# Performance work log

Hardware: AMD Instinct MI355X
Metric: run time of the kernel (lower is better)

## Reference

```python
import jax, jax.numpy as jnp
import numpy as np

B, T, D = 2, 4096, 2048
HK, HV = 16, 32            # key heads, value heads (gqa_factor = 2)
AK, UV = 128, 128          # key head dim A, value head dim U
KEY_DIM = HK * AK          # 2048
VALUE_DIM = HV * UV        # 4096
CONV_DIM = 2 * KEY_DIM + VALUE_DIM  # 8192
KCONV = 4
CHUNK = 64
EPS = 1e-6


def setup_inputs() -> dict:
    key = jax.random.key(0)
    ks = jax.random.split(key, 10)
    s = lambda d: 1.0 / np.sqrt(d)
    return {
        "hidden": jax.random.normal(ks[0], (B, T, D), jnp.float32),
        "W_qkv": jax.random.normal(ks[1], (D, CONV_DIM), jnp.float32) * s(D),
        "W_z": jax.random.normal(ks[2], (D, VALUE_DIM), jnp.float32) * s(D),
        "W_b": jax.random.normal(ks[3], (D, HV), jnp.float32) * s(D),
        "W_a": jax.random.normal(ks[4], (D, HV), jnp.float32) * s(D),
        "conv_weight": jax.random.normal(ks[5], (CONV_DIM, KCONV), jnp.float32) * s(KCONV),
        "dt_bias": jnp.ones((HV,), jnp.float32),
        "A_log": jnp.log(jax.random.uniform(ks[6], (HV,), jnp.float32) * 16.0 + 1e-4),
        "norm_w": jnp.ones((UV,), jnp.float32),
        "W_out": jax.random.normal(ks[7], (VALUE_DIM, D), jnp.float32) * s(VALUE_DIM),
    }


def _l2norm(x, eps=1e-6):
    return x * jax.lax.rsqrt((x * x).sum(axis=-1, keepdims=True) + eps)


def _chunk_gated_delta_rule(q, k, v, g, beta, chunk_size=CHUNK):
    # inputs: q,k (B,T,Hv,A) l2-normalized below; v (B,T,Hv,U); g,beta (B,T,Hv)
    q = _l2norm(q)
    k = _l2norm(k)
    q, k, v = [x.transpose(0, 2, 1, 3).astype(jnp.float32) for x in (q, k, v)]
    beta = beta.transpose(0, 2, 1).astype(jnp.float32)
    g = g.transpose(0, 2, 1).astype(jnp.float32)
    Bs, H, Tt, A = k.shape
    U = v.shape[-1]
    pad = (chunk_size - Tt % chunk_size) % chunk_size
    if pad:
        q = jnp.pad(q, ((0, 0), (0, 0), (0, pad), (0, 0)))
        k = jnp.pad(k, ((0, 0), (0, 0), (0, pad), (0, 0)))
        v = jnp.pad(v, ((0, 0), (0, 0), (0, pad), (0, 0)))
        beta = jnp.pad(beta, ((0, 0), (0, 0), (0, pad)))
        g = jnp.pad(g, ((0, 0), (0, 0), (0, pad)))
    total = Tt + pad
    J = total // chunk_size
    q = q * (A ** -0.5)
    vb = v * beta[..., None]
    kb = k * beta[..., None]
    rs = lambda x, d: x.reshape(Bs, H, J, chunk_size, d)
    qj, kj, kbj = rs(q, A), rs(k, A), rs(kb, A)
    vbj = rs(vb, U)
    gj = jnp.cumsum(g.reshape(Bs, H, J, chunk_size), axis=-1)
    tril = jnp.tril(jnp.ones((chunk_size, chunk_size), jnp.float32))
    decay = jnp.exp((gj[..., :, None] - gj[..., None, :]) * tril) * tril
    upper = jnp.triu(jnp.ones((chunk_size, chunk_size), bool))
    attn = -(jnp.einsum('BHJLA,BHJMA->BHJLM', kbj, kj) * decay)
    attn = jnp.where(upper, 0.0, attn)

    def correction_step(i, a):  # sequential UT transform over rows
        row = a[..., i, :]
        return a.at[..., i, :].set(row + jnp.einsum('...j,...jk->...k', row, a))

    attn = jax.lax.fori_loop(1, chunk_size, correction_step, attn)
    attn = attn + jnp.eye(chunk_size, dtype=jnp.float32)
    v_corr = jnp.einsum('BHJLM,BHJMU->BHJLU', attn, vbj)
    k_cd = jnp.einsum('BHJLM,BHJMA->BHJLA', attn, kbj * jnp.exp(gj)[..., None])
    upper1 = jnp.triu(jnp.ones((chunk_size, chunk_size), bool), k=1)

    def chunk_step(st, j):  # st: (B,H,A,U) recurrent state
        qc, kc = qj[:, :, j], kj[:, :, j]
        vc, gc, kcd = v_corr[:, :, j], gj[:, :, j], k_cd[:, :, j]
        dm = decay[:, :, j]
        intra = jnp.einsum('BHLA,BHMA->BHLM', qc, kc) * dm
        intra = jnp.where(upper1, 0.0, intra)
        v_new = vc - jnp.einsum('BHLA,BHAU->BHLU', kcd, st)
        inter = jnp.exp(gc)[..., None] * jnp.einsum('BHLA,BHAU->BHLU', qc, st)
        out_c = inter + jnp.einsum('BHLM,BHMU->BHLU', intra, v_new)
        k_dec = kc * jnp.exp(gc[:, :, -1:] - gc)[..., None]
        st = st * jnp.exp(gc[:, :, -1])[..., None, None] + jnp.einsum('BHMA,BHMU->BHAU', k_dec, v_new)
        return st, out_c

    st0 = jnp.zeros((Bs, H, A, U), jnp.float32)
    _, outs = jax.lax.scan(chunk_step, st0, jnp.arange(J))
    out = outs.transpose(1, 2, 0, 3, 4).reshape(Bs, H, total, U)[:, :, :Tt]
    return out.transpose(0, 2, 1, 3)  # (B,T,H,U)


def _forward(hidden, W_qkv, W_z, W_b, W_a, conv_weight, dt_bias, A_log, norm_w, W_out):
    Bs, Tl, _ = hidden.shape
    mixed = (hidden @ W_qkv).transpose(0, 2, 1)  # (B, C, T)
    z = hidden @ W_z                              # (B, T, value_dim)
    b = hidden @ W_b                              # (B, T, Hv)
    a = hidden @ W_a                              # (B, T, Hv)
    # causal depthwise conv1d (kernel KCONV) + SiLU
    xp = jnp.pad(mixed, ((0, 0), (0, 0), (KCONV - 1, 0)))
    conv = sum(conv_weight[None, :, kk:kk + 1] * xp[:, :, kk:kk + Tl] for kk in range(KCONV))
    mixed = jax.nn.silu(conv).transpose(0, 2, 1)  # (B, T, C)
    q, k, v = jnp.split(mixed, [KEY_DIM, 2 * KEY_DIM], axis=-1)
    q = q.reshape(Bs, Tl, HK, AK)
    k = k.reshape(Bs, Tl, HK, AK)
    v = v.reshape(Bs, Tl, HV, UV)
    beta = jax.nn.sigmoid(b)
    g = -jnp.exp(A_log.astype(jnp.float32)) * jax.nn.softplus(a.astype(jnp.float32) + dt_bias)
    gqa = HV // HK
    q = jnp.repeat(q, gqa, axis=2)  # matches broadcast_to+reshape interleaving
    k = jnp.repeat(k, gqa, axis=2)
    core = _chunk_gated_delta_rule(q, k, v, g, beta)  # (B,T,Hv,U)
    # gated RMSNorm per value head (Mamba2/Qwen3-Next style: gate then norm)
    x = core.reshape(-1, UV)
    zf = z.reshape(-1, UV).astype(jnp.float32)
    xg = x * jax.nn.silu(zf)
    normed = norm_w * (xg * jax.lax.rsqrt((xg * xg).mean(-1, keepdims=True) + EPS))
    return normed.reshape(Bs, Tl, VALUE_DIM).astype(hidden.dtype) @ W_out


def reference(hidden, W_qkv, W_z, W_b, W_a, conv_weight, dt_bias, A_log, norm_w, W_out):
    return _forward(hidden, W_qkv, W_z, W_b, W_a, conv_weight, dt_bias, A_log, norm_w, W_out)
```

## Files before the change

### kernel.cpp

```cpp
#include <hip/hip_runtime.h>

#define B_   2
#define T_   4096
#define D_   2048
#define HV_  32
#define AK_  128
#define UV_  128
#define KD_  2048
#define VD_  4096
#define CD_  8192
#define CHK  64
#define NCH  (T_/CHK)

typedef __attribute__((ext_vector_type(4))) float  f32x4;
typedef __attribute__((ext_vector_type(8))) short  short8;
typedef __attribute__((ext_vector_type(4))) short  short4b;
typedef __attribute__((ext_vector_type(8))) unsigned short u16x8;
typedef __attribute__((ext_vector_type(4))) unsigned short u16x4;

__device__ __forceinline__ float bf2f(unsigned short u) {
  return __uint_as_float(((unsigned)u) << 16);
}
__device__ __forceinline__ unsigned short f2bf(float f) {
  unsigned u = __float_as_uint(f);
  return (unsigned short)((u + 0x7fffu + ((u >> 16) & 1u)) >> 16);
}
__device__ __forceinline__ void gload16(const void* g, void* l) {
  __builtin_amdgcn_global_load_lds((const __attribute__((address_space(1))) void*)g,
                                   (__attribute__((address_space(3))) void*)l, 16, 0, 0);
}

__global__ __launch_bounds__(256) void k_transpose(const float* __restrict__ src,
                                                   unsigned short* __restrict__ dst,
                                                   int K, int N) {
  __shared__ float tile[32][33];
  int k0 = blockIdx.x * 32, n0 = blockIdx.y * 32;
  int tx = threadIdx.x, ty = threadIdx.y;
  #pragma unroll
  for (int i = 0; i < 32; i += 8)
    tile[ty + i][tx] = src[(size_t)(k0 + ty + i) * N + n0 + tx];
  __syncthreads();
  #pragma unroll
  for (int i = 0; i < 32; i += 8)
    dst[(size_t)(n0 + ty + i) * K + k0 + tx] = f2bf(tile[tx][ty + i]);
}

__device__ __forceinline__ void storeC(float* p, float v) { *p = v; }
__device__ __forceinline__ void storeC(unsigned short* p, float v) { *p = f2bf(v); }

template <bool AGL, typename CT>
__global__ __launch_bounds__(256, 2) void k_gemm(const void* __restrict__ Av,
                                                 const unsigned short* __restrict__ BT,
                                                 CT* __restrict__ C, int M, int N, int K) {
  __shared__ __attribute__((aligned(16))) short As[128 * 32];
  __shared__ __attribute__((aligned(16))) short Bs[256 * 32];
  const int tid  = threadIdx.x;
  const size_t bm = (size_t)blockIdx.x * 128;
  const size_t bn = (size_t)blockIdx.y * 256;
  const int lane = tid & 63;
  const int wave = tid >> 6;
  const int wm = (wave >> 1) * 64;
  const int wn = (wave & 1) * 64;
  const int fr = lane & 15;
  const int kg = lane >> 4;
  const int lr = lane >> 2, lc8 = (lane & 3) * 8;
  const short* gb = (const short*)BT + (bn + wave * 64 + lr) * (size_t)K + lc8;
  short* lB = &Bs[wave * 64 * 32];
  const short* gab = (const short*)Av + (bm + wave * 32 + lr) * (size_t)K + lc8;
  short* lA = &As[wave * 32 * 32];

  f32x4 acc[4][8];
  #pragma unroll
  for (int i = 0; i < 4; ++i)
    #pragma unroll
    for (int j2 = 0; j2 < 8; ++j2) acc[i][j2] = (f32x4){0.f, 0.f, 0.f, 0.f};

  for (int kt = 0; kt < K; kt += 32) {
    __syncthreads();
    gload16(gb + kt, lB);
    gload16(gb + kt + (size_t)16 * K, lB + 16 * 32);
    gload16(gb + kt + (size_t)32 * K, lB + 32 * 32);
    gload16(gb + kt + (size_t)48 * K, lB + 48 * 32);
    if constexpr (AGL) {
      gload16(gab + kt, lA);
      gload16(gab + kt + (size_t)16 * K, lA + 16 * 32);
    } else {
      const float* Ag = (const float*)Av + bm * (size_t)K;
      #pragma unroll
      for (int s = 0; s < 4; ++s) {
        int ch = s * 256 + tid;
        int r = ch >> 3, c4 = (ch & 7) * 4;
        float4 v = *(const float4*)(Ag + (size_t)r * K + kt + c4);
        short4b sv = { (short)f2bf(v.x), (short)f2bf(v.y), (short)f2bf(v.z), (short)f2bf(v.w) };
        *(short4b*)&As[r * 32 + c4] = sv;
      }
    }
    __syncthreads();
    short8 af[4], bfr[8];
    #pragma unroll
    for (int mi = 0; mi < 4; ++mi) af[mi] = *(const short8*)&As[(wm + mi*16 + fr)*32 + kg*8];
    #pragma unroll
    for (int ni = 0; ni < 4; ++ni) {
      bfr[ni]     = *(const short8*)&Bs[(wn + ni*16 + fr)*32 + kg*8];
      bfr[4 + ni] = *(const short8*)&Bs[(128 + wn + ni*16 + fr)*32 + kg*8];
    }
    #pragma unroll
    for (int mi = 0; mi < 4; ++mi)
      #pragma unroll
      for (int ni = 0; ni < 8; ++ni)
        acc[mi][ni] = __builtin_amdgcn_mfma_f32_16x16x32_bf16(af[mi], bfr[ni], acc[mi][ni], 0, 0, 0);
  }
  #pragma unroll
  for (int mi = 0; mi < 4; ++mi)
    #pragma unroll
    for (int ni = 0; ni < 8; ++ni) {
      size_t row = bm + wm + mi * 16 + kg * 4;
      size_t col = bn + (ni >= 4 ? 128 : 0) + wn + (ni & 3) * 16 + fr;
      #pragma unroll
      for (int e = 0; e < 4; ++e) storeC(&C[(row + e) * (size_t)N + col], acc[mi][ni][e]);
    }
}

__global__ __launch_bounds__(256) void k_beta_g(const float* __restrict__ hidden,
                                                const float* __restrict__ Wb,
                                                const float* __restrict__ Wa,
                                                const float* __restrict__ dt_bias,
                                                const float* __restrict__ A_log,
                                                float* __restrict__ betab,
                                                float* __restrict__ gbuf) {
  const int tid = threadIdx.x;
  const int r = tid >> 5, hh = tid & 31;
  const size_t bt = (size_t)blockIdx.x * 8 + r;
  const float* hrow = hidden + bt * D_;
  float sb = 0.f, sa = 0.f;
  for (int d = 0; d < D_; ++d) {
    float hv = hrow[d];
    sb += hv * Wb[d * 32 + hh];
    sa += hv * Wa[d * 32 + hh];
  }
  float beta = 1.f / (1.f + expf(-sb));
  float xg = sa + dt_bias[hh];
  float sp = (xg > 20.f) ? xg : log1pf(expf(xg));
  float g = -expf(A_log[hh]) * sp;
  int b = (int)(bt >> 12);
  int t = (int)(bt & (T_ - 1));
  size_t o = ((size_t)b * HV_ + hh) * T_ + t;
  betab[o] = beta;
  gbuf[o] = g;
}

__global__ __launch_bounds__(256) void k_qkv(const unsigned short* __restrict__ mqk,
                                             const float* __restrict__ cw,
                                             unsigned short* __restrict__ qn,
                                             unsigned short* __restrict__ kn) {
  const int row = blockIdx.x;
  const int b = row >> 12, t = row & (T_ - 1);
  const int tid = threadIdx.x;
  const int c0 = tid * 16;
  float4 w[16];
  #pragma unroll
  for (int e = 0; e < 16; ++e) w[e] = *(const float4*)&cw[(size_t)(c0 + e) * 4];
  float acc[16];
  #pragma unroll
  for (int e = 0; e < 16; ++e) acc[e] = 0.f;
  #pragma unroll
  for (int p = 0; p < 4; ++p) {
    int ts = t - 3 + p;
    if (ts < 0) continue;
    const unsigned short* src = mqk + (size_t)(b * T_ + ts) * 4096 + c0;
    u16x8 v0 = *(const u16x8*)src;
    u16x8 v1 = *(const u16x8*)(src + 8);
    #pragma unroll
    for (int e = 0; e < 8; ++e) {
      acc[e]     += bf2f(v0[e]) * ((const float*)&w[e])[p];
      acc[8 + e] += bf2f(v1[e]) * ((const float*)&w[8 + e])[p];
    }
  }
  float s = 0.f;
  #pragma unroll
  for (int e = 0; e < 16; ++e) {
    float x = acc[e];
    x = x / (1.f + expf(-x));
    acc[e] = x;
    s += x * x;
  }
  s += __shfl_xor(s, 1); s += __shfl_xor(s, 2); s += __shfl_xor(s, 4);
  float sc = rsqrtf(s + 1e-6f);
  bool isq = (c0 < KD_);
  if (isq) sc *= 0.08838834764831845f;
  int ch = isq ? c0 : (c0 - KD_);
  int hk = ch >> 7, cc = ch & 127;
  unsigned short* dst = (isq ? qn : kn) + ((size_t)(b * 16 + hk) * T_ + t) * 128 + cc;
  u16x8 o0, o1;
  #pragma unroll
  for (int e = 0; e < 8; ++e) { o0[e] = f2bf(acc[e] * sc); o1[e] = f2bf(acc[8 + e] * sc); }
  *(u16x8*)dst = o0;
  *(u16x8*)(dst + 8) = o1;
}

__global__ __launch_bounds__(256) void k_prep(const unsigned short* __restrict__ kn,
                                              const float* __restrict__ gbuf,
                                              const float* __restrict__ betab,
                                              unsigned short* __restrict__ Tg,
                                              unsigned short* __restrict__ knT,
                                              float* __restrict__ gjc) {
  __shared__ __attribute__((aligned(16))) unsigned short kl[CHK][136];
  __shared__ float L[CHK][65];
  __shared__ float W1[CHK][65];
  __shared__ float gj[CHK], bet[CHK];
  const int tid = threadIdx.x;
  const int blk = blockIdx.x;
  const int j = blk & 63, h = (blk >> 6) & 31, b = blk >> 11;
  const int hk = h >> 1;
  const int t0 = j * CHK;
  const int lane = tid & 63, wv = tid >> 6;
  const int fr = lane & 15, kg = lane >> 4;
  const int ty = tid >> 4, tx = tid & 15;

  const unsigned short* ksrc = kn + ((size_t)(b * 16 + hk) * T_ + t0) * 128;
  #pragma unroll
  for (int p = 0; p < 4; ++p) {
    int id = p * 256 + tid;
    int r = id >> 4, c = (id & 15) * 8;
    *(u16x8*)&kl[r][c] = *(const u16x8*)(ksrc + (size_t)r * 128 + c);
  }
  if (tid < 64) {
    float gval = gbuf[((size_t)b * HV_ + h) * T_ + t0 + tid];
    #pragma unroll
    for (int off = 1; off < 64; off <<= 1) {
      float o = __shfl_up(gval, off);
      if (tid >= off) gval += o;
    }
    gj[tid] = gval;
    gjc[((size_t)(b * HV_ + h) * NCH + j) * 64 + tid] = gval;
    bet[tid] = betab[((size_t)b * HV_ + h) * T_ + t0 + tid];
  }
  __syncthreads();

  if ((h & 1) == 0) {
    unsigned short* kd = knT + ((size_t)(b * 16 + hk) * NCH + j) * 8192;
    int a = tid >> 1, l0 = (tid & 1) * 32;
    u16x8 o[4];
    #pragma unroll
    for (int i = 0; i < 32; ++i) ((unsigned short*)o)[i] = kl[l0 + i][a];
    #pragma unroll
    for (int p = 0; p < 4; ++p) *(u16x8*)(kd + a * 64 + l0 + p * 8) = o[p];
  }

  {
    const int s0 = 16 * wv;
    f32x4 ag[4];
    #pragma unroll
    for (int mt = 0; mt < 4; ++mt) ag[mt] = (f32x4){0.f, 0.f, 0.f, 0.f};
    #pragma unroll
    for (int ks = 0; ks < 4; ++ks) {
      short8 af = *(const short8*)&kl[s0 + fr][ks * 32 + kg * 8];
      #pragma unroll
      for (int mt = 0; mt < 4; ++mt) {
        short8 bfv = *(const short8*)&kl[mt * 16 + fr][ks * 32 + kg * 8];
        ag[mt] = __builtin_amdgcn_mfma_f32_16x16x32_bf16(af, bfv, ag[mt], 0, 0, 0);
      }
    }
    #pragma unroll
    for (int mt = 0; mt < 4; ++mt)
      #pragma unroll
      for (int e = 0; e < 4; ++e) {
        int l = s0 + kg * 4 + e, m = mt * 16 + fr;
        L[l][m] = (l > m) ? (-bet[l] * ag[mt][e] * expf(gj[l] - gj[m])) : 0.f;
      }
  }
  __syncthreads();
  for (int i = tid; i < CHK * CHK; i += 256) { int l = i >> 6, m = i & 63; W1[l][m] = L[l][m]; }
  __syncthreads();

  #pragma unroll
  for (int dk = 1; dk <= 5; ++dk) {
    const int p2 = 1 << (dk - 1);
    float s4[4][4];
    #pragma unroll
    for (int i = 0; i < 4; ++i)
      #pragma unroll
      for (int c = 0; c < 4; ++c) s4[i][c] = 0.f;
    {
      const int hi = 16 * wv + 15 - p2;
      for (int jm = p2; jm <= hi; ++jm) {
        float wl[4], wr[4];
        #pragma unroll
        for (int i = 0; i < 4; ++i) wl[i] = W1[ty * 4 + i][jm];
        #pragma unroll
        for (int c = 0; c < 4; ++c) wr[c] = W1[jm][tx * 4 + c];
        #pragma unroll
        for (int i = 0; i < 4; ++i)
          #pragma unroll
          for (int c = 0; c < 4; ++c) s4[i][c] += wl[i] * wr[c];
      }
    }
    __syncthreads();
    #pragma unroll
    for (int i = 0; i < 4; ++i)
      #pragma unroll
      for (int c = 0; c < 4; ++c) W1[ty * 4 + i][tx * 4 + c] = s4[i][c];
    __syncthreads();
    float pu[4][4];
    #pragma unroll
    for (int i = 0; i < 4; ++i)
      #pragma unroll
      for (int c = 0; c < 4; ++c) pu[i][c] = L[ty * 4 + i][tx * 4 + c] + W1[ty * 4 + i][tx * 4 + c];
    {
      const int hi = 16 * wv + 14;
      for (int jm = p2 * 2; jm <= hi; ++jm) {
        float pl[4], wr[4];
        #pragma unroll
        for (int i = 0; i < 4; ++i) pl[i] = L[ty * 4 + i][jm];
        #pragma unroll
        for (int c = 0; c < 4; ++c) wr[c] = W1[jm][tx * 4 + c];
        #pragma unroll
        for (int i = 0; i < 4; ++i)
          #pragma unroll
          for (int c = 0; c < 4; ++c) pu[i][c] += pl[i] * wr[c];
      }
    }
    __syncthreads();
    #pragma unroll
    for (int i = 0; i < 4; ++i)
      #pragma unroll
      for (int c = 0; c < 4; ++c) L[ty * 4 + i][tx * 4 + c] = pu[i][c];
    __syncthreads();
  }
  unsigned short* td = Tg + (size_t)blk * 4096;
  #pragma unroll
  for (int pp = 0; pp < 2; ++pp) {
    int id = pp * 256 + tid;
    int l = id >> 3, m8 = (id & 7) * 8;
    u16x8 o;
    #pragma unroll
    for (int e = 0; e < 8; ++e) {
      float v = L[l][m8 + e] + ((l == m8 + e) ? 1.f : 0.f);
      o[e] = f2bf(v);
    }
    *(u16x8*)(td + (size_t)l * 64 + m8) = o;
  }
}

__global__ __launch_bounds__(256) void k_scan(const unsigned short* __restrict__ qn,
                                              const unsigned short* __restrict__ kn,
                                              const unsigned short* __restrict__ mv,
                                              const unsigned short* __restrict__ Tg,
                                              const unsigned short* __restrict__ knT,
                                              const float* __restrict__ gjc,
                                              const float* __restrict__ betab,
                                              const float* __restrict__ cw,
                                              unsigned short* __restrict__ xout) {
  __shared__ __attribute__((aligned(16))) unsigned short kl[CHK][136], ql[CHK][136];
  __shared__ __attribute__((aligned(16))) unsigned short Ubuf[9216];
  __shared__ float ST[16][132];
  __shared__ __attribute__((aligned(16))) unsigned short SbT[16][136];
  __shared__ __attribute__((aligned(16))) unsigned short vbT[16][72], vnT[16][72], vndT[16][72];
  __shared__ float gj[CHK], bet[CHK], eg[CHK], edec[CHK], beg[CHK];

  unsigned short (*Tl)[72]   = (unsigned short(*)[72])(&Ubuf[0]);
  unsigned short (*intr)[72] = (unsigned short(*)[72])(&Ubuf[4608]);

  const int tid = threadIdx.x;
  const int blk = blockIdx.x;
  const int xcd  = blk & 7;
  const int slot = blk >> 3;
  const int g    = xcd + 8 * (slot >> 4);
  const int wgrp = slot & 15;
  const int b  = g >> 4;
  const int hk = g & 15;
  const int h  = hk * 2 + (wgrp >> 3);
  const int us = wgrp & 7;
  const int u0 = us * 16;
  const int lane = tid & 63, wv = tid >> 6;
  const int fr = lane & 15, kg = lane >> 4;
  const int s0 = 16 * wv;

  const int cvl = tid >> 2, c4 = (tid & 3) * 4;
  float4 wv4[4];
  #pragma unroll
  for (int i = 0; i < 4; ++i)
    wv4[i] = *(const float4*)&cw[(size_t)(2 * KD_ + h * 128 + u0 + c4 + i) * 4];

  for (int i = tid; i < 16 * 132; i += 256) (&ST[0][0])[i] = 0.f;

  const unsigned short* qsrc = qn + (size_t)(b * 16 + hk) * T_ * 128;
  const unsigned short* ksrc = kn + (size_t)(b * 16 + hk) * T_ * 128;
  const unsigned short* tsrc = Tg + (size_t)((b * 32 + h) * 64) * 4096;
  const unsigned short* knsrc = knT + (size_t)(b * 16 + hk) * NCH * 8192;
  const float* gsrc = gjc + (size_t)(b * 32 + h) * 4096;
  const float* bsrc = betab + ((size_t)b * HV_ + h) * T_;
  __syncthreads();

  for (int j = 0; j < NCH; ++j) {
    const int t0 = j * CHK;
    short8 kr[2][2];
    #pragma unroll
    for (int t2 = 0; t2 < 2; ++t2) {
      int a0 = wv * 32 + t2 * 16;
      #pragma unroll
      for (int ks = 0; ks < 2; ++ks)
        kr[t2][ks] = *(const short8*)(knsrc + (size_t)j * 8192 + (a0 + fr) * 64 + ks * 32 + kg * 8);
    }
    #pragma unroll
    for (int p = 0; p < 4; ++p) {
      int id = p * 256 + tid;
      int r = id >> 4, c = (id & 15) * 8;
      *(u16x8*)&kl[r][c] = *(const u16x8*)(ksrc + (size_t)(t0 + r) * 128 + c);
      *(u16x8*)&ql[r][c] = *(const u16x8*)(qsrc + (size_t)(t0 + r) * 128 + c);
    }
    #pragma unroll
    for (int p = 0; p < 2; ++p) {
      int id = p * 256 + tid;
      int r = id >> 3, c = (id & 7) * 8;
      *(u16x8*)&Tl[r][c] = *(const u16x8*)(tsrc + (size_t)j * 4096 + r * 64 + c);
    }
    if (tid < 64) {
      gj[tid] = gsrc[j * 64 + tid];
      bet[tid] = bsrc[t0 + tid];
    }
    __syncthreads();
    if (tid < 64) {
      float gl = gj[63];
      float e = expf(gj[tid]);
      eg[tid] = e;
      edec[tid] = expf(gl - gj[tid]);
      beg[tid] = bet[tid] * e;
    }
    {
      float a4[4] = {0.f, 0.f, 0.f, 0.f};
      #pragma unroll
      for (int p = 0; p < 4; ++p) {
        int ts = t0 + cvl - 3 + p;
        if (ts >= 0) {
          u16x4 vv = *(const u16x4*)(mv + (size_t)(b * T_ + ts) * 4096 + h * 128 + u0 + c4);
          #pragma unroll
          for (int i = 0; i < 4; ++i) a4[i] += bf2f(vv[i]) * ((const float*)&wv4[i])[p];
        }
      }
      float be = bet[cvl];
      #pragma unroll
      for (int i = 0; i < 4; ++i) {
        float x = a4[i];
        x = x / (1.f + expf(-x)) * be;
        vbT[c4 + i][cvl] = f2bf(x);
      }
    }
    {
      int u = tid >> 4, a8 = (tid & 15) * 8;
      u16x8 o;
      #pragma unroll
      for (int e = 0; e < 8; ++e) o[e] = f2bf(ST[u][a8 + e]);
      *(u16x8*)&SbT[u][a8] = o;
    }
    __syncthreads();

    {
      f32x4 ag[4];
      #pragma unroll
      for (int mt = 0; mt < 4; ++mt) ag[mt] = (f32x4){0.f, 0.f, 0.f, 0.f};
      #pragma unroll
      for (int ks = 0; ks < 4; ++ks) {
        short8 af = *(const short8*)&ql[s0 + fr][ks * 32 + kg * 8];
        #pragma unroll
        for (int mt = 0; mt < 4; ++mt) {
          short8 bfv = *(const short8*)&kl[mt * 16 + fr][ks * 32 + kg * 8];
          ag[mt] = __builtin_amdgcn_mfma_f32_16x16x32_bf16(af, bfv, ag[mt], 0, 0, 0);
        }
      }
      #pragma unroll
      for (int mt = 0; mt < 4; ++mt)
        #pragma unroll
        for (int e = 0; e < 4; ++e) {
          int l = s0 + kg * 4 + e, m = mt * 16 + fr;
          float v = (l >= m) ? (ag[mt][e] * expf(gj[l] - gj[m])) : 0.f;
          intr[l][m] = f2bf(v);
        }
    }
    {
      f32x4 a1 = (f32x4){0.f, 0.f, 0.f, 0.f};
      #pragma unroll
      for (int ks = 0; ks < 4; ++ks) {
        short8 af = *(const short8*)&kl[s0 + fr][ks * 32 + kg * 8];
        short8 bfv = *(const short8*)&SbT[fr][ks * 32 + kg * 8];
        a1 = __builtin_amdgcn_mfma_f32_16x16x32_bf16(af, bfv, a1, 0, 0, 0);
      }
      #pragma unroll
      for (int e = 0; e < 4; ++e) {
        int l = s0 + kg * 4 + e;
        float vm = bf2f(vbT[fr][l]) - beg[l] * a1[e];
        vbT[fr][l] = f2bf(vm);
      }
    }
    __syncthreads();
    {
      f32x4 a2 = (f32x4){0.f, 0.f, 0.f, 0.f};
      #pragma unroll
      for (int ks = 0; ks < 2; ++ks) {
        short8 af = *(const short8*)&Tl[s0 + fr][ks * 32 + kg * 8];
        short8 bfv = *(const short8*)&vbT[fr][ks * 32 + kg * 8];
        a2 = __builtin_amdgcn_mfma_f32_16x16x32_bf16(af, bfv, a2, 0, 0, 0);
      }
      #pragma unroll
      for (int e = 0; e < 4; ++e) {
        int l = s0 + kg * 4 + e;
        vnT[fr][l]  = f2bf(a2[e]);
        vndT[fr][l] = f2bf(a2[e] * edec[l]);
      }
    }
    __syncthreads();
    {
      f32x4 ai = (f32x4){0.f, 0.f, 0.f, 0.f};
      f32x4 aq = (f32x4){0.f, 0.f, 0.f, 0.f};
      #pragma unroll
      for (int ks = 0; ks < 2; ++ks) {
        short8 af = *(const short8*)&intr[s0 + fr][ks * 32 + kg * 8];
        short8 bfv = *(const short8*)&vnT[fr][ks * 32 + kg * 8];
        ai = __builtin_amdgcn_mfma_f32_16x16x32_bf16(af, bfv, ai, 0, 0, 0);
      }
      #pragma unroll
      for (int ks = 0; ks < 4; ++ks) {
        short8 af = *(const short8*)&ql[s0 + fr][ks * 32 + kg * 8];
        short8 bfv = *(const short8*)&SbT[fr][ks * 32 + kg * 8];
        aq = __builtin_amdgcn_mfma_f32_16x16x32_bf16(af, bfv, aq, 0, 0, 0);
      }
      #pragma unroll
      for (int e = 0; e < 4; ++e) {
        int l = s0 + kg * 4 + e;
        float o = eg[l] * aq[e] + ai[e];
        xout[((size_t)(b * T_ + t0 + l) * HV_ + h) * UV_ + u0 + fr] = f2bf(o);
      }
    }
    {
      float egl = eg[63];
      #pragma unroll
      for (int t2 = 0; t2 < 2; ++t2) {
        int a0 = wv * 32 + t2 * 16;
        f32x4 cf;
        #pragma unroll
        for (int e = 0; e < 4; ++e) cf[e] = ST[kg * 4 + e][a0 + fr] * egl;
        #pragma unroll
        for (int ks = 0; ks < 2; ++ks) {
          short8 af = *(const short8*)&vndT[fr][ks * 32 + kg * 8];
          cf = __builtin_amdgcn_mfma_f32_16x16x32_bf16(af, kr[t2][ks], cf, 0, 0, 0);
        }
        #pragma unroll
        for (int e = 0; e < 4; ++e) ST[kg * 4 + e][a0 + fr] = cf[e];
      }
    }
    __syncthreads();
  }
}

__global__ __launch_bounds__(256) void k_gate_norm(const unsigned short* __restrict__ x,
                                                   const unsigned short* __restrict__ z,
                                                   const float* __restrict__ nw,
                                                   unsigned short* __restrict__ out) {
  const int row = blockIdx.x * 4 + (threadIdx.x >> 6);
  const int lane = threadIdx.x & 63;
  const unsigned short* xp = x + (size_t)row * UV_;
  const unsigned short* zp = z + (size_t)row * UV_;
  float x0 = bf2f(xp[lane]), x1 = bf2f(xp[lane + 64]);
  float z0 = bf2f(zp[lane]), z1 = bf2f(zp[lane + 64]);
  float g0 = x0 * (z0 / (1.f + expf(-z0)));
  float g1 = x1 * (z1 / (1.f + expf(-z1)));
  float s = g0 * g0 + g1 * g1;
  #pragma unroll
  for (int off = 32; off > 0; off >>= 1) s += __shfl_xor(s, off);
  float r = rsqrtf(s * (1.f / UV_) + 1e-6f);
  out[(size_t)row * UV_ + lane]      = f2bf(nw[lane] * g0 * r);
  out[(size_t)row * UV_ + lane + 64] = f2bf(nw[lane + 64] * g1 * r);
}

extern "C" void kernel_launch(void* const* d_in, const int* in_sizes, int n_in,
                              void* d_out, int out_size, void* d_ws, size_t ws_size,
                              hipStream_t stream) {
  (void)in_sizes; (void)n_in; (void)out_size; (void)ws_size;
  const float* hidden  = (const float*)d_in[0];
  const float* W_qkv   = (const float*)d_in[1];
  const float* W_z     = (const float*)d_in[2];
  const float* W_b     = (const float*)d_in[3];
  const float* W_a     = (const float*)d_in[4];
  const float* conv_w  = (const float*)d_in[5];
  const float* dt_bias = (const float*)d_in[6];
  const float* A_log   = (const float*)d_in[7];
  const float* norm_w  = (const float*)d_in[8];
  const float* W_out   = (const float*)d_in[9];
  float* out = (float*)d_out;

  const size_t MB = 1048576ull;
  char* w = (char*)d_ws;
  unsigned short* wqkvT = (unsigned short*)(w);
  unsigned short* Tg    = (unsigned short*)(w);
  unsigned short* mqk   = (unsigned short*)(w + 32 * MB);
  unsigned short* xcore = (unsigned short*)(w + 32 * MB);
  unsigned short* mv    = (unsigned short*)(w + 96 * MB);
  unsigned short* normed= (unsigned short*)(w + 96 * MB);
  unsigned short* qn    = (unsigned short*)(w + 160 * MB);
  unsigned short* zb    = (unsigned short*)(w + 160 * MB);
  unsigned short* knT   = (unsigned short*)(w + 192 * MB);
  unsigned short* kn    = (unsigned short*)(w + 224 * MB);
  unsigned short* wzT   = (unsigned short*)(w + 224 * MB);
  unsigned short* woutT = (unsigned short*)(w + 240 * MB);
  float*          betab = (float*)(w + 288 * MB);
  float*          gbuf  = (float*)(w + 289 * MB);
  float*          gjc   = (float*)(w + 290 * MB);

  k_transpose<<<dim3(D_ / 32, CD_ / 32), dim3(32, 8), 0, stream>>>(W_qkv, wqkvT, D_, CD_);
  k_gemm<false, unsigned short><<<dim3(64, 16), 256, 0, stream>>>(hidden, wqkvT, mqk, 8192, 4096, 2048);
  k_gemm<false, unsigned short><<<dim3(64, 16), 256, 0, stream>>>(hidden, wqkvT + (size_t)4096 * 2048, mv, 8192, 4096, 2048);
  k_beta_g<<<dim3(B_ * T_ / 8), 256, 0, stream>>>(hidden, W_b, W_a, dt_bias, A_log, betab, gbuf);
  k_qkv<<<dim3(B_ * T_), 256, 0, stream>>>(mqk, conv_w, qn, kn);
  k_prep<<<dim3(B_ * HV_ * NCH), 256, 0, stream>>>(kn, gbuf, betab, Tg, knT, gjc);
  k_scan<<<dim3(B_ * HV_ * 8), 256, 0, stream>>>(qn, kn, mv, Tg, knT, gjc, betab, conv_w, xcore);
  k_transpose<<<dim3(D_ / 32, VD_ / 32), dim3(32, 8), 0, stream>>>(W_z, wzT, D_, VD_);
  k_gemm<false, unsigned short><<<dim3(64, 16), 256, 0, stream>>>(hidden, wzT, zb, 8192, 4096, 2048);
  k_transpose<<<dim3(VD_ / 32, D_ / 32), dim3(32, 8), 0, stream>>>(W_out, woutT, VD_, D_);
  k_gate_norm<<<dim3(B_ * T_ * HV_ / 4), 256, 0, stream>>>(xcore, zb, norm_w, normed);
  k_gemm<true, float><<<dim3(64, 8), 256, 0, stream>>>(normed, woutT, out, 8192, 2048, 4096);
}
```

Before: 1.777 ms.

## Prefetch next chunk's q/k/T/g/beta/v into registers during recurrence

Software-pipelines the chunk recurrence kernel: the global loads of the next chunk's q, k, T matrix, gate, beta and conv inputs are issued into registers at the start of the current iteration and written to shared memory after the state update. This hides global memory latency behind the MFMA work of the sequential chunk loop. It adds register pressure and an extra barrier per iteration, which may lower occupancy.

```diff
diff --git a/kernel.cpp b/kernel.cpp
--- a/kernel.cpp
+++ b/kernel.cpp
@@ -390,6 +390,45 @@
   const unsigned short* knsrc = knT + (size_t)(b * 16 + hk) * NCH * 8192;
   const float* gsrc = gjc + (size_t)(b * 32 + h) * 4096;
   const float* bsrc = betab + ((size_t)b * HV_ + h) * T_;
+
+  const int sr  = (tid + 0) >> 4;
+  const int rr = tid >> 4, cc8 = (tid & 15) * 8;
+  const int tr = tid >> 3, tc8 = (tid & 7) * 8;
+
+  u16x8 krg[4], qrg[4], trg[2];
+  u16x4 vld[4];
+  float g_r = 0.f, b_r = 0.f;
+
+  #pragma unroll
+  for (int p = 0; p < 4; ++p) {
+    int r = p * 16 + rr;
+    krg[p] = *(const u16x8*)(ksrc + (size_t)r * 128 + cc8);
+    qrg[p] = *(const u16x8*)(qsrc + (size_t)r * 128 + cc8);
+  }
+  #pragma unroll
+  for (int p = 0; p < 2; ++p) {
+    int r = p * 32 + tr;
+    trg[p] = *(const u16x8*)(tsrc + (size_t)r * 64 + tc8);
+  }
+  if (tid < 64) { g_r = gsrc[tid]; b_r = bsrc[tid]; }
+  #pragma unroll
+  for (int p = 0; p < 4; ++p) {
+    int ts = cvl - 3 + p;
+    vld[p] = (ts >= 0) ? *(const u16x4*)(mv + (size_t)(b * T_ + ts) * 4096 + h * 128 + u0 + c4)
+                       : (u16x4){0, 0, 0, 0};
+  }
+  #pragma unroll
+  for (int p = 0; p < 4; ++p) {
+    int r = p * 16 + rr;
+    *(u16x8*)&kl[r][cc8] = krg[p];
+    *(u16x8*)&ql[r][cc8] = qrg[p];
+  }
+  #pragma unroll
+  for (int p = 0; p < 2; ++p) {
+    int r = p * 32 + tr;
+    *(u16x8*)&Tl[r][tc8] = trg[p];
+  }
+  if (tid < 64) { gj[tid] = g_r; bet[tid] = b_r; }
   __syncthreads();
 
   for (int j = 0; j < NCH; ++j) {
@@ -402,24 +441,21 @@
       for (int ks = 0; ks < 2; ++ks)
         kr[t2][ks] = *(const short8*)(knsrc + (size_t)j * 8192 + (a0 + fr) * 64 + ks * 32 + kg * 8);
     }
-    #pragma unroll
-    for (int p = 0; p < 4; ++p) {
-      int id = p * 256 + tid;
-      int r = id >> 4, c = (id & 15) * 8;
-      *(u16x8*)&kl[r][c] = *(const u16x8*)(ksrc + (size_t)(t0 + r) * 128 + c);
-      *(u16x8*)&ql[r][c] = *(const u16x8*)(qsrc + (size_t)(t0 + r) * 128 + c);
-    }
-    #pragma unroll
-    for (int p = 0; p < 2; ++p) {
-      int id = p * 256 + tid;
-      int r = id >> 3, c = (id & 7) * 8;
-      *(u16x8*)&Tl[r][c] = *(const u16x8*)(tsrc + (size_t)j * 4096 + r * 64 + c);
-    }
-    if (tid < 64) {
-      gj[tid] = gsrc[j * 64 + tid];
-      bet[tid] = bsrc[t0 + tid];
-    }
-    __syncthreads();
+    if (j + 1 < NCH) {
+      const int t1 = t0 + CHK;
+      #pragma unroll
+      for (int p = 0; p < 4; ++p) {
+        int r = p * 16 + rr;
+        krg[p] = *(const u16x8*)(ksrc + (size_t)(t1 + r) * 128 + cc8);
+        qrg[p] = *(const u16x8*)(qsrc + (size_t)(t1 + r) * 128 + cc8);
+      }
+      #pragma unroll
+      for (int p = 0; p < 2; ++p) {
+        int r = p * 32 + tr;
+        trg[p] = *(const u16x8*)(tsrc + (size_t)(j + 1) * 4096 + r * 64 + tc8);
+      }
+      if (tid < 64) { g_r = gsrc[(j + 1) * 64 + tid]; b_r = bsrc[t1 + tid]; }
+    }
     if (tid < 64) {
       float gl = gj[63];
       float e = expf(gj[tid]);
@@ -430,20 +466,22 @@
     {
       float a4[4] = {0.f, 0.f, 0.f, 0.f};
       #pragma unroll
-      for (int p = 0; p < 4; ++p) {
-        int ts = t0 + cvl - 3 + p;
-        if (ts >= 0) {
-          u16x4 vv = *(const u16x4*)(mv + (size_t)(b * T_ + ts) * 4096 + h * 128 + u0 + c4);
-          #pragma unroll
-          for (int i = 0; i < 4; ++i) a4[i] += bf2f(vv[i]) * ((const float*)&wv4[i])[p];
-        }
-      }
+      for (int p = 0; p < 4; ++p)
+        #pragma unroll
+        for (int i = 0; i < 4; ++i) a4[i] += bf2f(vld[p][i]) * ((const float*)&wv4[i])[p];
       float be = bet[cvl];
       #pragma unroll
       for (int i = 0; i < 4; ++i) {
         float x = a4[i];
         x = x / (1.f + expf(-x)) * be;
         vbT[c4 + i][cvl] = f2bf(x);
+      }
+    }
+    if (j + 1 < NCH) {
+      #pragma unroll
+      for (int p = 0; p < 4; ++p) {
+        int ts = t0 + CHK + cvl - 3 + p;
+        vld[p] = *(const u16x4*)(mv + (size_t)(b * T_ + ts) * 4096 + h * 128 + u0 + c4);
       }
     }
     {
@@ -547,6 +585,21 @@
         #pragma unroll
         for (int e = 0; e < 4; ++e) ST[kg * 4 + e][a0 + fr] = cf[e];
       }
+    }
+    __syncthreads();
+    if (j + 1 < NCH) {
+      #pragma unroll
+      for (int p = 0; p < 4; ++p) {
+        int r = p * 16 + rr;
+        *(u16x8*)&kl[r][cc8] = krg[p];
+        *(u16x8*)&ql[r][cc8] = qrg[p];
+      }
+      #pragma unroll
+      for (int p = 0; p < 2; ++p) {
+        int r = p * 32 + tr;
+        *(u16x8*)&Tl[r][tc8] = trg[p];
+      }
+      if (tid < 64) { gj[tid] = g_r; bet[tid] = b_r; }
     }
     __syncthreads();
   }
```

After: 1.702 ms. 4.2% less time.
